# Performance work log

Measured on AMD Instinct MI355X. Metric: run time of the kernel, lower is better.

## Reference

```python
import jax, jax.numpy as jnp
import numpy as np

DIM = 1024
HEADS = 8


def setup_inputs() -> dict:
    key = jax.random.key(0)
    ks = jax.random.split(key, 8)
    b, n, m, nc, d = 2, 1024, 4, 1024, DIM
    x = jax.random.normal(ks[0], (b, n, d), dtype=jnp.float32)
    context = jax.random.normal(ks[1], (b, m, nc, d), dtype=jnp.float32)
    doc_similarities = jax.random.normal(ks[2], (b, m), dtype=jnp.float32)
    # learned params (Linear weights stored as [in, out] for x @ W)
    s = 1.0 / np.sqrt(d)
    Wq = jax.random.uniform(ks[3], (d, d), minval=-s, maxval=s, dtype=jnp.float32)
    Wkv = jax.random.uniform(ks[4], (d, 2 * d), minval=-s, maxval=s, dtype=jnp.float32)
    Wout = jax.random.uniform(ks[5], (d, d), minval=-s, maxval=s, dtype=jnp.float32)
    bout = jax.random.uniform(ks[6], (d,), minval=-s, maxval=s, dtype=jnp.float32)
    beta = jnp.array(1.0, dtype=jnp.float32)
    return {"x": x, "context": context, "doc_similarities": doc_similarities,
            "Wq": Wq, "Wkv": Wkv, "beta": beta, "Wout": Wout, "bout": bout}


def reference(x, context, doc_similarities, Wq, Wkv, beta, Wout, bout):
    b, n, dim = x.shape
    h = HEADS
    hd = dim // h
    scale = dim ** -0.5
    m, nc = context.shape[1], context.shape[2]

    # q: [b, h, n, hd]
    q = (x @ Wq).reshape(b, n, h, hd).transpose(0, 2, 1, 3)

    # flatten docs: [b, m*nc, dim]
    ctx = context.reshape(b, m * nc, dim)
    # doc similarity bias, repeated per token within each doc: [b, m*nc]
    sim = jnp.repeat(doc_similarities, nc, axis=1) * beta

    kv = ctx @ Wkv  # [b, L, 2*dim]
    k, v = jnp.split(kv, 2, axis=-1)
    k = k.reshape(b, m * nc, h, hd).transpose(0, 2, 1, 3)  # [b, h, L, hd]
    v = v.reshape(b, m * nc, h, hd).transpose(0, 2, 1, 3)

    dots = jnp.einsum('bhid,bhjd->bhij', q, k) * scale
    dots = dots + sim[:, None, None, :]
    attn = jax.nn.softmax(dots, axis=-1)
    out = jnp.einsum('bhij,bhjd->bhid', attn, v)
    out = out.transpose(0, 2, 1, 3).reshape(b, n, dim)
    return out @ Wout + bout
```

## Files before the change

kernel.cpp:

```cpp
#include <hip/hip_runtime.h>
#include <stdint.h>

typedef __attribute__((ext_vector_type(4))) float f32x4;
typedef __attribute__((ext_vector_type(8))) __bf16 bf16x8;
typedef __attribute__((ext_vector_type(2))) unsigned int u32x2;

__device__ __forceinline__ uint16_t f2bf(float f) {
  uint32_t u = __builtin_bit_cast(uint32_t, f);
  u += 0x7FFFu + ((u >> 16) & 1u);
  return (uint16_t)(u >> 16);
}

__device__ __forceinline__ float bf2f(uint16_t u) {
  uint32_t v = ((uint32_t)u) << 16;
  return __builtin_bit_cast(float, v);
}

__device__ __forceinline__ uint32_t cvtpk_bf16(float lo, float hi) {
  uint32_t r;
  asm("v_cvt_pk_bf16_f32 %0, %1, %2" : "=v"(r) : "v"(lo), "v"(hi));
  return r;
}

__device__ __forceinline__ void swap_half32(uint32_t& a, uint32_t& b) {
#if __has_builtin(__builtin_amdgcn_permlane32_swap)
  u32x2 r = __builtin_amdgcn_permlane32_swap(a, b, false, false);
  a = r[0]; b = r[1];
#else
  int lane = __builtin_amdgcn_mbcnt_hi(~0u, __builtin_amdgcn_mbcnt_lo(~0u, 0));
  uint32_t ax = (uint32_t)__shfl_xor((int)a, 32, 64);
  uint32_t bx = (uint32_t)__shfl_xor((int)b, 32, 64);
  uint32_t an = (lane < 32) ? a : bx;
  uint32_t bn = (lane < 32) ? ax : b;
  a = an; b = bn;
#endif
}

__device__ __forceinline__ void swap_half16(uint32_t& a, uint32_t& b) {
#if __has_builtin(__builtin_amdgcn_permlane16_swap)
  u32x2 r = __builtin_amdgcn_permlane16_swap(a, b, false, false);
  a = r[0]; b = r[1];
#else
  int lane = __builtin_amdgcn_mbcnt_hi(~0u, __builtin_amdgcn_mbcnt_lo(~0u, 0));
  uint32_t ax = (uint32_t)__shfl_xor((int)a, 16, 64);
  uint32_t bx = (uint32_t)__shfl_xor((int)b, 16, 64);
  uint32_t an = ((lane & 16) == 0) ? a : bx;
  uint32_t bn = ((lane & 16) == 0) ? ax : b;
  a = an; b = bn;
#endif
}

__device__ __forceinline__ void load_lds16(const uint16_t* g, uint16_t* l) {
  __builtin_amdgcn_global_load_lds((const __attribute__((address_space(1))) void*)g,
                                   (__attribute__((address_space(3))) void*)l, 16, 0, 0);
}

__global__ __launch_bounds__(256) void k_prep(const float* __restrict__ x,
                                              const float* __restrict__ ctx,
                                              const float* __restrict__ Wq,
                                              const float* __restrict__ Wkv,
                                              const float* __restrict__ Wout,
                                              uint16_t* __restrict__ xb,
                                              uint16_t* __restrict__ ctxb,
                                              uint16_t* __restrict__ wqt,
                                              uint16_t* __restrict__ wkvt,
                                              uint16_t* __restrict__ woutt,
                                              float qscale) {
  __shared__ float tile[32][33];
  int id = blockIdx.x;
  int tid = threadIdx.x;
  if (id < 10240) {
    const float* in;
    uint16_t* out;
    int j = id * 256 + tid;
    if (j < 524288) { in = x; out = xb; }
    else            { in = ctx; out = ctxb; j -= 524288; }
    float4 v = ((const float4*)in)[j];
    union { uint16_t u[4]; uint64_t q; } o;
    o.u[0] = f2bf(v.x); o.u[1] = f2bf(v.y); o.u[2] = f2bf(v.z); o.u[3] = f2bf(v.w);
    ((uint64_t*)out)[j] = o.q;
    return;
  }
  id -= 10240;
  const float* W;
  uint16_t* Wt;
  int N, n0, k0;
  float sc = 1.0f;
  if (id < 1024)      { W = Wq;   Wt = wqt;   N = 1024; sc = qscale;
                        n0 = (id & 31) * 32; k0 = (id >> 5) * 32; }
  else if (id < 2048) { W = Wout; Wt = woutt; N = 1024; id -= 1024;
                        n0 = (id & 31) * 32; k0 = (id >> 5) * 32; }
  else                { W = Wkv;  Wt = wkvt;  N = 2048; id -= 2048;
                        n0 = (id & 63) * 32; k0 = (id >> 6) * 32; }
  int c = tid & 31, r0 = tid >> 5;
#pragma unroll
  for (int i = 0; i < 4; i++) {
    int r = r0 + i * 8;
    tile[r][c] = W[(size_t)(k0 + r) * N + n0 + c];
  }
  __syncthreads();
#pragma unroll
  for (int i = 0; i < 4; i++) {
    int r = r0 + i * 8;
    Wt[(size_t)(n0 + r) * 1024 + k0 + c] = f2bf(tile[c][r] * sc);
  }
}

__global__ __launch_bounds__(256, 4) void k_gemm_fused(const uint16_t* __restrict__ ctxb,
                                                       const uint16_t* __restrict__ wkvt,
                                                       const uint16_t* __restrict__ xb,
                                                       const uint16_t* __restrict__ wqt,
                                                       uint16_t* __restrict__ kb,
                                                       uint16_t* __restrict__ vtb,
                                                       uint16_t* __restrict__ qb) {
  __shared__ uint16_t smem[16384];
  const int K = 1024;
  const int tid = threadIdx.x;
  const int lane = tid & 63, w = tid >> 6;
  const int quad = lane >> 4, l16 = lane & 15;
  const int wr = (w >> 1) * 64, wc = (w & 1) * 64;
  int id = blockIdx.x;
  int bx, by, isQ;
  const uint16_t *Ab, *Bb;
  if (id < 1024) {
    isQ = 0;
    int xcd = id & 7, t = id >> 3;
    by = (xcd << 3) + (t & 7);
    bx = t >> 3;
    Ab = ctxb + (size_t)by * 128 * K;
    Bb = wkvt + (size_t)bx * 128 * K;
  } else {
    isQ = 1; id -= 1024;
    int xcd = id & 7, t = id >> 3;
    by = (xcd << 1) + (t & 1);
    bx = t >> 1;
    Ab = xb + (size_t)by * 128 * K;
    Bb = wqt + (size_t)bx * 128 * K;
  }
  f32x4 acc[4][4] = {};
  const int rA = tid >> 2, slotA = tid & 3;
  const int rA1 = rA + 64;
  const int segA0 = (slotA ^ ((rA + (rA >> 2)) & 3)) * 8;
  const int segA1 = (slotA ^ ((rA1 + (rA1 >> 2)) & 3)) * 8;
  const uint16_t* gA0 = Ab + (size_t)rA * K + segA0;
  const uint16_t* gA1 = Ab + (size_t)rA1 * K + segA1;
  const uint16_t* gB0 = Bb + (size_t)rA * K + segA0;
  const uint16_t* gB1 = Bb + (size_t)rA1 * K + segA1;
  load_lds16(gA0, smem + tid * 8);
  load_lds16(gA1, smem + (tid + 256) * 8);
  load_lds16(gB0, smem + (tid + 512) * 8);
  load_lds16(gB1, smem + (tid + 768) * 8);
  for (int t = 0; t < 32; ++t) {
    const uint16_t* la = smem + (t & 1) * 8192;
    const uint16_t* lb = la + 4096;
    if (t < 31) {
      uint16_t* ln = smem + ((t + 1) & 1) * 8192;
      const int k1 = (t + 1) * 32;
      load_lds16(gA0 + k1, ln + tid * 8);
      load_lds16(gA1 + k1, ln + (tid + 256) * 8);
      load_lds16(gB0 + k1, ln + (tid + 512) * 8);
      load_lds16(gB1 + k1, ln + (tid + 768) * 8);
      asm volatile("s_waitcnt vmcnt(4)\n\ts_barrier" ::: "memory");
    } else {
      asm volatile("s_waitcnt vmcnt(0)\n\ts_barrier" ::: "memory");
    }
    bf16x8 af[4], bfr[4];
#pragma unroll
    for (int i = 0; i < 4; i++) {
      int R = wr + i * 16 + l16;
      int s = quad ^ ((R + (R >> 2)) & 3);
      af[i] = *(const bf16x8*)&la[R * 32 + s * 8];
    }
#pragma unroll
    for (int j = 0; j < 4; j++) {
      int R = wc + j * 16 + l16;
      int s = quad ^ ((R + (R >> 2)) & 3);
      bfr[j] = *(const bf16x8*)&lb[R * 32 + s * 8];
    }
    __builtin_amdgcn_s_setprio(1);
#pragma unroll
    for (int i = 0; i < 4; i++)
#pragma unroll
      for (int j = 0; j < 4; j++)
        acc[i][j] = __builtin_amdgcn_mfma_f32_16x16x32_bf16(af[i], bfr[j], acc[i][j], 0, 0, 0);
    __builtin_amdgcn_s_setprio(0);
    asm volatile("s_barrier" ::: "memory");
  }
  __syncthreads();
  if (isQ) {
#pragma unroll
    for (int i = 0; i < 4; i++)
#pragma unroll
      for (int j = 0; j < 4; j++) {
        size_t row = (size_t)by * 128 + wr + i * 16 + quad * 4;
        size_t col = (size_t)bx * 128 + wc + j * 16 + l16;
#pragma unroll
        for (int r = 0; r < 4; r++)
          qb[(row + r) * 1024 + col] = f2bf(acc[i][j][r]);
      }
  } else if (bx < 8) {
#pragma unroll
    for (int i = 0; i < 4; i++)
#pragma unroll
      for (int j = 0; j < 4; j++) {
        int rowg = by * 128 + wr + i * 16 + quad * 4;
        int bb = rowg >> 12, l = rowg & 4095;
        int c = wc + j * 16 + l16;
        uint16_t* dst = kb + (((size_t)(bb * 8 + bx) * 4096 + l) * 128 + c);
#pragma unroll
        for (int r = 0; r < 4; r++)
          dst[r * 128] = f2bf(acc[i][j][r]);
      }
  } else {
    const int bh = (by >> 5) * 8 + (bx - 8);
    const int lbase = (by & 31) * 128;
    uint16_t* vdst = vtb + (size_t)bh * 524288;
#pragma unroll
    for (int half = 0; half < 2; half++) {
      if (wr == half * 64) {
#pragma unroll
        for (int i = 0; i < 4; i++)
#pragma unroll
          for (int j = 0; j < 4; j++) {
            int rowl = i * 16 + quad * 4;
            int col = wc + j * 16 + l16;
            union { uint64_t q; uint16_t u[4]; } pk;
#pragma unroll
            for (int r = 0; r < 4; r++) pk.u[r] = f2bf(acc[i][j][r]);
            *(uint64_t*)&smem[col * 72 + rowl] = pk.q;
          }
      }
      __syncthreads();
      {
        int col = tid >> 1, rseg = (tid & 1) * 32;
        const uint16_t* src = &smem[col * 72 + rseg];
        uint16_t* d = vdst + (size_t)col * 4096 + lbase + half * 64 + rseg;
#pragma unroll
        for (int k = 0; k < 4; k++)
          ((uint4*)d)[k] = *(const uint4*)&src[k * 8];
      }
      __syncthreads();
    }
  }
}

__global__ __launch_bounds__(256) void k_gemm64(const uint16_t* __restrict__ A,
                                                const uint16_t* __restrict__ Bt,
                                                float* __restrict__ Cf,
                                                const float* __restrict__ bias,
                                                int M, int N, int K) {
  __shared__ uint16_t smem[16384];
  const int tid = threadIdx.x;
  const int lane = tid & 63, w = tid >> 6;
  const int quad = lane >> 4, l16 = lane & 15;
  const int wr = (w >> 1) * 32, wc = (w & 1) * 32;
  const size_t tr0 = (size_t)blockIdx.y * 64, tc0 = (size_t)blockIdx.x * 64;
  f32x4 acc[2][2] = {};
  const int rS = tid >> 3, sS = tid & 7;
  const int seg = (sS ^ (rS & 7)) * 8;
  const uint16_t* Ab = A + tr0 * K;
  const uint16_t* Bb = Bt + tc0 * K;
  const uint16_t* gA0 = Ab + (size_t)rS * K + seg;
  const uint16_t* gA1 = Ab + (size_t)(rS + 32) * K + seg;
  const uint16_t* gB0 = Bb + (size_t)rS * K + seg;
  const uint16_t* gB1 = Bb + (size_t)(rS + 32) * K + seg;
  const int NT = K >> 6;
  load_lds16(gA0, smem + tid * 8);
  load_lds16(gA1, smem + (tid + 256) * 8);
  load_lds16(gB0, smem + (tid + 512) * 8);
  load_lds16(gB1, smem + (tid + 768) * 8);
  for (int t = 0; t < NT; ++t) {
    const uint16_t* la = smem + (t & 1) * 8192;
    const uint16_t* lb = la + 4096;
    if (t < NT - 1) {
      uint16_t* ln = smem + ((t + 1) & 1) * 8192;
      const int k1 = (t + 1) * 64;
      load_lds16(gA0 + k1, ln + tid * 8);
      load_lds16(gA1 + k1, ln + (tid + 256) * 8);
      load_lds16(gB0 + k1, ln + (tid + 512) * 8);
      load_lds16(gB1 + k1, ln + (tid + 768) * 8);
      asm volatile("s_waitcnt vmcnt(4)\n\ts_barrier" ::: "memory");
    } else {
      asm volatile("s_waitcnt vmcnt(0)\n\ts_barrier" ::: "memory");
    }
    __builtin_amdgcn_s_setprio(1);
#pragma unroll
    for (int sub = 0; sub < 2; sub++) {
      const int kk = sub * 4 + quad;
      bf16x8 af[2], bfr[2];
#pragma unroll
      for (int i = 0; i < 2; i++) {
        int R = wr + i * 16 + l16;
        af[i] = *(const bf16x8*)&la[R * 64 + (kk ^ (R & 7)) * 8];
      }
#pragma unroll
      for (int j = 0; j < 2; j++) {
        int R = wc + j * 16 + l16;
        bfr[j] = *(const bf16x8*)&lb[R * 64 + (kk ^ (R & 7)) * 8];
      }
#pragma unroll
      for (int i = 0; i < 2; i++)
#pragma unroll
        for (int j = 0; j < 2; j++)
          acc[i][j] = __builtin_amdgcn_mfma_f32_16x16x32_bf16(af[i], bfr[j], acc[i][j], 0, 0, 0);
    }
    __builtin_amdgcn_s_setprio(0);
    asm volatile("s_barrier" ::: "memory");
  }
#pragma unroll
  for (int i = 0; i < 2; i++) {
#pragma unroll
    for (int j = 0; j < 2; j++) {
      size_t row = tr0 + wr + i * 16 + quad * 4;
      size_t col = tc0 + wc + j * 16 + l16;
#pragma unroll
      for (int r = 0; r < 4; r++)
        Cf[(row + r) * N + col] = acc[i][j][r] + bias[col];
    }
  }
}

__global__ __launch_bounds__(256) void k_attn(const uint16_t* __restrict__ q,
                                              const uint16_t* __restrict__ kb,
                                              const uint16_t* __restrict__ vt,
                                              const float* __restrict__ sims,
                                              const float* __restrict__ beta,
                                              uint16_t* __restrict__ po,
                                              float* __restrict__ pl) {
  __shared__ uint16_t Kl[2][8192];
  __shared__ uint16_t Vl[2][8192];
  const int idx = blockIdx.x;
  const int qbx = idx >> 6, g = idx & 63;
  const int h = g >> 3, b = (g >> 2) & 1, sp = g & 3;
  const int q0 = qbx * 128;
  const int tid = threadIdx.x, lane = tid & 63, w = tid >> 6;
  const int quad = lane >> 4, l16 = lane & 15;
  const float wsplit =
      __builtin_amdgcn_exp2f(sims[b * 4 + sp] * beta[0] * 1.44269504f);

  union { uint32_t u[4]; bf16x8 v; } Oc;
#pragma unroll
  for (int j = 0; j < 4; j++) Oc.u[j] = 0x3F803F80u;
  const bf16x8 onesf = Oc.v;

  bf16x8 qf[2][4];
#pragma unroll
  for (int rb = 0; rb < 2; rb++) {
    const uint16_t* qrow =
        q + ((size_t)(b * 1024 + q0 + w * 32 + rb * 16 + l16)) * 1024 + h * 128 + quad * 8;
#pragma unroll
    for (int ks = 0; ks < 4; ks++) qf[rb][ks] = *(const bf16x8*)(qrow + ks * 32);
  }
  f32x4 o[2][8] = {};
  f32x4 o9[2] = {};

  const uint16_t* kptr = kb + ((size_t)(b * 8 + h) * 4096 + sp * 1024) * 128;
  const uint16_t* vptr = vt + ((size_t)(b * 8 + h) * 128) * 4096 + sp * 1024;

#pragma unroll
  for (int ii = 0; ii < 4; ii++) {
    int g2 = tid + ii * 256;
    int row = g2 >> 4, seg = (g2 & 15) ^ (row & 15);
    load_lds16(kptr + row * 128 + seg * 8, &Kl[0][g2 * 8]);
  }
#pragma unroll
  for (int ii = 0; ii < 4; ii++) {
    int g2 = tid + ii * 256;
    int row = g2 >> 3, seg = (g2 & 7) ^ (row & 7);
    load_lds16(vptr + (size_t)row * 4096 + seg * 8, &Vl[0][g2 * 8]);
  }

  for (int c = 0; c < 16; c++) {
    const uint16_t* Kc = Kl[c & 1];
    const uint16_t* Vc = Vl[c & 1];
    if (c < 15) {
      const uint16_t* kn = kptr + 64 * 128;
      const uint16_t* vn = vptr + 64;
      uint16_t* Kd = Kl[(c + 1) & 1];
      uint16_t* Vd = Vl[(c + 1) & 1];
#pragma unroll
      for (int ii = 0; ii < 4; ii++) {
        int g2 = tid + ii * 256;
        int row = g2 >> 4, seg = (g2 & 15) ^ (row & 15);
        load_lds16(kn + row * 128 + seg * 8, Kd + g2 * 8);
      }
#pragma unroll
      for (int ii = 0; ii < 4; ii++) {
        int g2 = tid + ii * 256;
        int row = g2 >> 3, seg = (g2 & 7) ^ (row & 7);
        load_lds16(vn + (size_t)row * 4096 + seg * 8, Vd + g2 * 8);
      }
      asm volatile("s_waitcnt vmcnt(8)\n\ts_barrier" ::: "memory");
    } else {
      asm volatile("s_waitcnt vmcnt(0)\n\ts_barrier" ::: "memory");
    }
#pragma unroll
    for (int kh = 0; kh < 2; kh++) {
      f32x4 s[2][2] = {{{0.f,0.f,0.f,0.f},{0.f,0.f,0.f,0.f}},
                       {{0.f,0.f,0.f,0.f},{0.f,0.f,0.f,0.f}}};
      __builtin_amdgcn_s_setprio(1);
#pragma unroll
      for (int nb2 = 0; nb2 < 2; nb2++) {
        const int nb = kh * 2 + nb2;
#pragma unroll
        for (int ks = 0; ks < 4; ks++) {
          bf16x8 kf = *(const bf16x8*)&Kc[(nb * 16 + l16) * 128 + (((ks * 4 + quad) ^ l16) * 8)];
          s[nb2][0] = __builtin_amdgcn_mfma_f32_16x16x32_bf16(kf, qf[0][ks], s[nb2][0], 0, 0, 0);
          s[nb2][1] = __builtin_amdgcn_mfma_f32_16x16x32_bf16(kf, qf[1][ks], s[nb2][1], 0, 0, 0);
        }
      }
      __builtin_amdgcn_s_setprio(0);
      bf16x8 pa[2];
#pragma unroll
      for (int qh = 0; qh < 2; qh++) {
        uint32_t a0 = cvtpk_bf16(__builtin_amdgcn_exp2f(s[0][qh][0]),
                                 __builtin_amdgcn_exp2f(s[0][qh][1]));
        uint32_t a1 = cvtpk_bf16(__builtin_amdgcn_exp2f(s[0][qh][2]),
                                 __builtin_amdgcn_exp2f(s[0][qh][3]));
        uint32_t b0 = cvtpk_bf16(__builtin_amdgcn_exp2f(s[1][qh][0]),
                                 __builtin_amdgcn_exp2f(s[1][qh][1]));
        uint32_t b1 = cvtpk_bf16(__builtin_amdgcn_exp2f(s[1][qh][2]),
                                 __builtin_amdgcn_exp2f(s[1][qh][3]));
        swap_half32(a0, b0);
        swap_half16(a0, b0);
        swap_half32(a1, b1);
        swap_half16(a1, b1);
        union { uint32_t u[4]; bf16x8 v; } pk_;
        pk_.u[0] = a0; pk_.u[1] = a1; pk_.u[2] = b0; pk_.u[3] = b1;
        pa[qh] = pk_.v;
      }
      const int sq = ((kh * 4 + quad) ^ (l16 & 7)) * 8;
      __builtin_amdgcn_s_setprio(1);
#pragma unroll
      for (int nb = 0; nb < 8; nb++) {
        bf16x8 vf = *(const bf16x8*)&Vc[(nb * 16 + l16) * 64 + sq];
        o[0][nb] = __builtin_amdgcn_mfma_f32_16x16x32_bf16(pa[0], vf, o[0][nb], 0, 0, 0);
        o[1][nb] = __builtin_amdgcn_mfma_f32_16x16x32_bf16(pa[1], vf, o[1][nb], 0, 0, 0);
      }
      o9[0] = __builtin_amdgcn_mfma_f32_16x16x32_bf16(pa[0], onesf, o9[0], 0, 0, 0);
      o9[1] = __builtin_amdgcn_mfma_f32_16x16x32_bf16(pa[1], onesf, o9[1], 0, 0, 0);
      __builtin_amdgcn_s_setprio(0);
    }
    asm volatile("s_barrier" ::: "memory");
    kptr += 64 * 128;
    vptr += 64;
  }
  const int rowbase = (sp * 16 + b * 8 + h) * 1024 + q0 + w * 32;
#pragma unroll
  for (int rb = 0; rb < 2; rb++)
#pragma unroll
    for (int r = 0; r < 4; r++) {
      int row = rowbase + rb * 16 + quad * 4 + r;
#pragma unroll
      for (int nb = 0; nb < 8; nb++)
        po[(size_t)row * 128 + nb * 16 + l16] = f2bf(o[rb][nb][r] * wsplit);
      if (l16 == 0)
        pl[row] = o9[rb][r] * wsplit;
    }
}

__global__ __launch_bounds__(256) void k_merge(const uint16_t* __restrict__ po,
                                               const float* __restrict__ pl,
                                               uint16_t* __restrict__ attb) {
  const int bq = blockIdx.x;
  const int b = bq >> 10, qi = bq & 1023;
  const int t = threadIdx.x;
  const int h = t >> 5, d0 = (t & 31) * 4;
  const int bh = b * 8 + h;
  float den = 0.f;
  float acc[4] = {0.f, 0.f, 0.f, 0.f};
#pragma unroll
  for (int s = 0; s < 4; s++) {
    den += pl[(s * 16 + bh) * 1024 + qi];
    union { uint64_t q; uint16_t u[4]; } v;
    v.q = *(const uint64_t*)&po[(((size_t)(s * 16 + bh)) * 1024 + qi) * 128 + d0];
#pragma unroll
    for (int j = 0; j < 4; j++) acc[j] += bf2f(v.u[j]);
  }
  const float inv = 1.0f / den;
  union { uint64_t q; uint16_t u[4]; } o;
#pragma unroll
  for (int j = 0; j < 4; j++) o.u[j] = f2bf(acc[j] * inv);
  *(uint64_t*)&attb[((size_t)(b * 1024 + qi)) * 1024 + h * 128 + d0] = o.q;
}

extern "C" void kernel_launch(void* const* d_in, const int* in_sizes, int n_in,
                              void* d_out, int out_size, void* d_ws, size_t ws_size,
                              hipStream_t stream) {
  (void)in_sizes; (void)n_in; (void)out_size; (void)ws_size;
  const float* x    = (const float*)d_in[0];
  const float* ctx  = (const float*)d_in[1];
  const float* sims = (const float*)d_in[2];
  const float* Wq   = (const float*)d_in[3];
  const float* Wkv  = (const float*)d_in[4];
  const float* beta = (const float*)d_in[5];
  const float* Wout = (const float*)d_in[6];
  const float* bout = (const float*)d_in[7];
  float* out = (float*)d_out;

  char* ws = (char*)d_ws;
  uint16_t* xb    = (uint16_t*)(ws + 0);
  uint16_t* ctxb  = (uint16_t*)(ws + (4u << 20));
  uint16_t* wqt   = (uint16_t*)(ws + (20u << 20));
  uint16_t* wkvt  = (uint16_t*)(ws + (22u << 20));
  uint16_t* kb    = (uint16_t*)(ws + (32u << 20));
  uint16_t* vtb   = (uint16_t*)(ws + (48u << 20));
  float*    pl    = (float*)   (ws + (64u << 20));
  uint16_t* woutt = (uint16_t*)(ws + (68u << 20));
  uint16_t* qb    = (uint16_t*)(ws + (70u << 20));
  uint16_t* attb  = (uint16_t*)(ws + (74u << 20));
  uint16_t* po = (uint16_t*)(ws + 0);

  const float LOG2E = 1.44269504f;
  const float qscale = 0.03125f * LOG2E;

  k_prep<<<14336, 256, 0, stream>>>(x, ctx, Wq, Wkv, Wout, xb, ctxb, wqt, wkvt, woutt, qscale);
  k_gemm_fused<<<1152, 256, 0, stream>>>(ctxb, wkvt, xb, wqt, kb, vtb, qb);
  k_attn<<<512, 256, 0, stream>>>(qb, kb, vtb, sims, beta, po, pl);
  k_merge<<<2048, 256, 0, stream>>>(po, pl, attb);
  k_gemm64<<<dim3(16, 32), 256, 0, stream>>>(attb, woutt, out, bout, 2048, 1024, 1024);
}
```

Baseline: 208.1 us.

## Split fused GEMM into 256x256 KV GEMM with 4-stage pipeline and separate Q GEMM

The KV projection moves to its own kernel with 256x256 tiles, 512 threads, a 4-buffer LDS ring (128 KB) and a 3-deep prefetch, which raises arithmetic intensity and hides global latency. The Q projection becomes a separate launch reusing the old 128x128 code. This adds one kernel launch and serializes Q after KV instead of sharing a grid. The KV grid is 256 blocks at one block per CU, so wave-level occupancy drops and the epilogue writes through a larger LDS transpose.

```diff
diff --git a/kernel.cpp b/kernel.cpp
--- a/kernel.cpp
+++ b/kernel.cpp
@@ -106,13 +106,125 @@
   }
 }
 
-__global__ __launch_bounds__(256, 4) void k_gemm_fused(const uint16_t* __restrict__ ctxb,
-                                                       const uint16_t* __restrict__ wkvt,
-                                                       const uint16_t* __restrict__ xb,
-                                                       const uint16_t* __restrict__ wqt,
-                                                       uint16_t* __restrict__ kb,
-                                                       uint16_t* __restrict__ vtb,
-                                                       uint16_t* __restrict__ qb) {
+__global__ __launch_bounds__(512, 1) void k_gemm_kv(const uint16_t* __restrict__ ctxb,
+                                                    const uint16_t* __restrict__ wkvt,
+                                                    uint16_t* __restrict__ kb,
+                                                    uint16_t* __restrict__ vtb) {
+  __shared__ uint16_t smem[65536];
+  const int K = 1024;
+  const int tid = threadIdx.x;
+  const int lane = tid & 63, w = tid >> 6;
+  const int quad = lane >> 4, l16 = lane & 15;
+  const int wm = w >> 2, wn = w & 3;
+  const int wr = wm * 128, wc = wn * 64;
+  int id = blockIdx.x;
+  int xcd = id & 7, t0 = id >> 3;
+  int by = xcd + 8 * (t0 & 3);
+  int bx = t0 >> 2;
+  const uint16_t* Ab = ctxb + (size_t)by * 256 * K;
+  const uint16_t* Bb = wkvt + (size_t)bx * 256 * K;
+  f32x4 acc[8][4] = {};
+  const int rS = tid >> 2, sS = tid & 3;
+  const int rS1 = rS + 128;
+  const int seg0 = (sS ^ ((rS + (rS >> 2)) & 3)) * 8;
+  const int seg1 = (sS ^ ((rS1 + (rS1 >> 2)) & 3)) * 8;
+  const uint16_t* gA0 = Ab + (size_t)rS * K + seg0;
+  const uint16_t* gA1 = Ab + (size_t)rS1 * K + seg1;
+  const uint16_t* gB0 = Bb + (size_t)rS * K + seg0;
+  const uint16_t* gB1 = Bb + (size_t)rS1 * K + seg1;
+#define KV_STAGE(kt, buf)                                        \
+  {                                                              \
+    uint16_t* ba_ = smem + (buf) * 16384;                        \
+    const int k0_ = (kt) * 32;                                   \
+    load_lds16(gA0 + k0_, ba_ + tid * 8);                        \
+    load_lds16(gA1 + k0_, ba_ + 4096 + tid * 8);                 \
+    load_lds16(gB0 + k0_, ba_ + 8192 + tid * 8);                 \
+    load_lds16(gB1 + k0_, ba_ + 12288 + tid * 8);                \
+  }
+  KV_STAGE(0, 0)
+  KV_STAGE(1, 1)
+  KV_STAGE(2, 2)
+  for (int t = 0; t < 32; ++t) {
+    if (t < 30)      asm volatile("s_waitcnt vmcnt(8)\n\ts_barrier" ::: "memory");
+    else if (t == 30) asm volatile("s_waitcnt vmcnt(4)\n\ts_barrier" ::: "memory");
+    else             asm volatile("s_waitcnt vmcnt(0)\n\ts_barrier" ::: "memory");
+    if (t < 29) KV_STAGE(t + 3, (t + 3) & 3)
+    const uint16_t* la = smem + (t & 3) * 16384;
+    const uint16_t* lb = la + 8192;
+    bf16x8 af[8], bfr[4];
+#pragma unroll
+    for (int i = 0; i < 8; i++) {
+      int R = wr + i * 16 + l16;
+      int s = quad ^ ((R + (R >> 2)) & 3);
+      af[i] = *(const bf16x8*)&la[R * 32 + s * 8];
+    }
+#pragma unroll
+    for (int j = 0; j < 4; j++) {
+      int R = wc + j * 16 + l16;
+      int s = quad ^ ((R + (R >> 2)) & 3);
+      bfr[j] = *(const bf16x8*)&lb[R * 32 + s * 8];
+    }
+    __builtin_amdgcn_s_setprio(1);
+#pragma unroll
+    for (int i = 0; i < 8; i++)
+#pragma unroll
+      for (int j = 0; j < 4; j++)
+        acc[i][j] = __builtin_amdgcn_mfma_f32_16x16x32_bf16(af[i], bfr[j], acc[i][j], 0, 0, 0);
+    __builtin_amdgcn_s_setprio(0);
+  }
+#undef KV_STAGE
+  __syncthreads();
+  if (bx < 4) {
+#pragma unroll
+    for (int i = 0; i < 8; i++)
+#pragma unroll
+      for (int j = 0; j < 4; j++) {
+        int rowg = by * 256 + wr + i * 16 + quad * 4;
+        int bb = rowg >> 12, l = rowg & 4095;
+        int colg = bx * 256 + wc + j * 16 + l16;
+        int h = colg >> 7, c = colg & 127;
+        uint16_t* dst = kb + (((size_t)(bb * 8 + h) * 4096 + l) * 128 + c);
+#pragma unroll
+        for (int r = 0; r < 4; r++)
+          dst[r * 128] = f2bf(acc[i][j][r]);
+      }
+  } else {
+    const int vh = bx - 4;
+    const int bb = by >> 4;
+    const int lb0 = (by & 15) * 256;
+#pragma unroll
+    for (int hh = 0; hh < 2; hh++) {
+      if ((wn >> 1) == hh) {
+#pragma unroll
+        for (int i = 0; i < 8; i++)
+#pragma unroll
+          for (int j = 0; j < 4; j++) {
+            int d = (wn & 1) * 64 + j * 16 + l16;
+            int rowl = wr + i * 16 + quad * 4;
+            union { uint64_t q; uint16_t u[4]; } pk;
+#pragma unroll
+            for (int r = 0; r < 4; r++) pk.u[r] = f2bf(acc[i][j][r]);
+            *(uint64_t*)&smem[d * 264 + rowl] = pk.q;
+          }
+      }
+      __syncthreads();
+      {
+        const int bh = bb * 8 + vh * 2 + hh;
+        const int d = tid >> 2, ls = (tid & 3) * 64;
+        const uint16_t* src = &smem[d * 264 + ls];
+        uint16_t* vd = vtb + (size_t)bh * 524288 + (size_t)d * 4096 + lb0 + ls;
+#pragma unroll
+        for (int k = 0; k < 8; k++)
+          ((uint4*)vd)[k] = *(const uint4*)&src[k * 8];
+      }
+      __syncthreads();
+    }
+  }
+}
+
+__global__ __launch_bounds__(256, 4) void k_gemm_q(const uint16_t* __restrict__ xb,
+                                                   const uint16_t* __restrict__ wqt,
+                                                   uint16_t* __restrict__ qb) {
   __shared__ uint16_t smem[16384];
   const int K = 1024;
   const int tid = threadIdx.x;
@@ -120,23 +232,11 @@
   const int quad = lane >> 4, l16 = lane & 15;
   const int wr = (w >> 1) * 64, wc = (w & 1) * 64;
   int id = blockIdx.x;
-  int bx, by, isQ;
-  const uint16_t *Ab, *Bb;
-  if (id < 1024) {
-    isQ = 0;
-    int xcd = id & 7, t = id >> 3;
-    by = (xcd << 3) + (t & 7);
-    bx = t >> 3;
-    Ab = ctxb + (size_t)by * 128 * K;
-    Bb = wkvt + (size_t)bx * 128 * K;
-  } else {
-    isQ = 1; id -= 1024;
-    int xcd = id & 7, t = id >> 3;
-    by = (xcd << 1) + (t & 1);
-    bx = t >> 1;
-    Ab = xb + (size_t)by * 128 * K;
-    Bb = wqt + (size_t)bx * 128 * K;
-  }
+  int xcd = id & 7, t = id >> 3;
+  int by = (xcd << 1) + (t & 1);
+  int bx = t >> 1;
+  const uint16_t* Ab = xb + (size_t)by * 128 * K;
+  const uint16_t* Bb = wqt + (size_t)bx * 128 * K;
   f32x4 acc[4][4] = {};
   const int rA = tid >> 2, slotA = tid & 3;
   const int rA1 = rA + 64;
@@ -150,12 +250,12 @@
   load_lds16(gA1, smem + (tid + 256) * 8);
   load_lds16(gB0, smem + (tid + 512) * 8);
   load_lds16(gB1, smem + (tid + 768) * 8);
-  for (int t = 0; t < 32; ++t) {
-    const uint16_t* la = smem + (t & 1) * 8192;
+  for (int t2 = 0; t2 < 32; ++t2) {
+    const uint16_t* la = smem + (t2 & 1) * 8192;
     const uint16_t* lb = la + 4096;
-    if (t < 31) {
-      uint16_t* ln = smem + ((t + 1) & 1) * 8192;
-      const int k1 = (t + 1) * 32;
+    if (t2 < 31) {
+      uint16_t* ln = smem + ((t2 + 1) & 1) * 8192;
+      const int k1 = (t2 + 1) * 32;
       load_lds16(gA0 + k1, ln + tid * 8);
       load_lds16(gA1 + k1, ln + (tid + 256) * 8);
       load_lds16(gB0 + k1, ln + (tid + 512) * 8);
@@ -186,62 +286,16 @@
     __builtin_amdgcn_s_setprio(0);
     asm volatile("s_barrier" ::: "memory");
   }
-  __syncthreads();
-  if (isQ) {
-#pragma unroll
-    for (int i = 0; i < 4; i++)
-#pragma unroll
-      for (int j = 0; j < 4; j++) {
-        size_t row = (size_t)by * 128 + wr + i * 16 + quad * 4;
-        size_t col = (size_t)bx * 128 + wc + j * 16 + l16;
-#pragma unroll
-        for (int r = 0; r < 4; r++)
-          qb[(row + r) * 1024 + col] = f2bf(acc[i][j][r]);
-      }
-  } else if (bx < 8) {
-#pragma unroll
-    for (int i = 0; i < 4; i++)
-#pragma unroll
-      for (int j = 0; j < 4; j++) {
-        int rowg = by * 128 + wr + i * 16 + quad * 4;
-        int bb = rowg >> 12, l = rowg & 4095;
-        int c = wc + j * 16 + l16;
-        uint16_t* dst = kb + (((size_t)(bb * 8 + bx) * 4096 + l) * 128 + c);
-#pragma unroll
-        for (int r = 0; r < 4; r++)
-          dst[r * 128] = f2bf(acc[i][j][r]);
-      }
-  } else {
-    const int bh = (by >> 5) * 8 + (bx - 8);
-    const int lbase = (by & 31) * 128;
-    uint16_t* vdst = vtb + (size_t)bh * 524288;
-#pragma unroll
-    for (int half = 0; half < 2; half++) {
-      if (wr == half * 64) {
-#pragma unroll
-        for (int i = 0; i < 4; i++)
-#pragma unroll
-          for (int j = 0; j < 4; j++) {
-            int rowl = i * 16 + quad * 4;
-            int col = wc + j * 16 + l16;
-            union { uint64_t q; uint16_t u[4]; } pk;
-#pragma unroll
-            for (int r = 0; r < 4; r++) pk.u[r] = f2bf(acc[i][j][r]);
-            *(uint64_t*)&smem[col * 72 + rowl] = pk.q;
-          }
-      }
-      __syncthreads();
-      {
-        int col = tid >> 1, rseg = (tid & 1) * 32;
-        const uint16_t* src = &smem[col * 72 + rseg];
-        uint16_t* d = vdst + (size_t)col * 4096 + lbase + half * 64 + rseg;
-#pragma unroll
-        for (int k = 0; k < 4; k++)
-          ((uint4*)d)[k] = *(const uint4*)&src[k * 8];
-      }
-      __syncthreads();
-    }
-  }
+#pragma unroll
+  for (int i = 0; i < 4; i++)
+#pragma unroll
+    for (int j = 0; j < 4; j++) {
+      size_t row = (size_t)by * 128 + wr + i * 16 + quad * 4;
+      size_t col = (size_t)bx * 128 + wc + j * 16 + l16;
+#pragma unroll
+      for (int r = 0; r < 4; r++)
+        qb[(row + r) * 1024 + col] = f2bf(acc[i][j][r]);
+    }
 }
 
 __global__ __launch_bounds__(256) void k_gemm64(const uint16_t* __restrict__ A,
@@ -515,7 +569,8 @@
   const float qscale = 0.03125f * LOG2E;
 
   k_prep<<<14336, 256, 0, stream>>>(x, ctx, Wq, Wkv, Wout, xb, ctxb, wqt, wkvt, woutt, qscale);
-  k_gemm_fused<<<1152, 256, 0, stream>>>(ctxb, wkvt, xb, wqt, kb, vtb, qb);
+  k_gemm_kv<<<256, 512, 0, stream>>>(ctxb, wkvt, kb, vtb);
+  k_gemm_q<<<128, 256, 0, stream>>>(xb, wqt, qb);
   k_attn<<<512, 256, 0, stream>>>(qb, kb, vtb, sims, beta, po, pl);
   k_merge<<<2048, 256, 0, stream>>>(po, pl, attb);
   k_gemm64<<<dim3(16, 32), 256, 0, stream>>>(attb, woutt, out, bout, 2048, 1024, 1024);
```

Result: slower. 217.3 us (+4.4%).

## Fuse split-KV merge into attention kernel via last-block atomic counter

Applied to the files above, without the earlier changes.

Removes the separate merge kernel launch. Each attention block now increments a per-(query block, head, batch) counter after writing its partial output. The block that finishes last for a group reduces the four partials and writes the normalized bf16 result. The counters are zeroed in the prep kernel. This saves one launch and some DRAM round-trip latency, but adds atomics and fences, and the tail merge work runs on only a quarter of the blocks with a less coalesced per-thread access pattern.

```diff
diff --git a/kernel.cpp b/kernel.cpp
--- a/kernel.cpp
+++ b/kernel.cpp
@@ -65,10 +65,12 @@
                                               uint16_t* __restrict__ wqt,
                                               uint16_t* __restrict__ wkvt,
                                               uint16_t* __restrict__ woutt,
+                                              int* __restrict__ ctr,
                                               float qscale) {
   __shared__ float tile[32][33];
   int id = blockIdx.x;
   int tid = threadIdx.x;
+  if (id == 0 && tid < 128) ctr[tid] = 0;
   if (id < 10240) {
     const float* in;
     uint16_t* out;
@@ -326,9 +328,12 @@
                                               const float* __restrict__ sims,
                                               const float* __restrict__ beta,
                                               uint16_t* __restrict__ po,
-                                              float* __restrict__ pl) {
+                                              float* __restrict__ pl,
+                                              uint16_t* __restrict__ attb,
+                                              int* __restrict__ ctr) {
   __shared__ uint16_t Kl[2][8192];
   __shared__ uint16_t Vl[2][8192];
+  __shared__ int last_flag;
   const int idx = blockIdx.x;
   const int qbx = idx >> 6, g = idx & 63;
   const int h = g >> 3, b = (g >> 2) & 1, sp = g & 3;
@@ -457,31 +462,37 @@
       if (l16 == 0)
         pl[row] = o9[rb][r] * wsplit;
     }
-}
-
-__global__ __launch_bounds__(256) void k_merge(const uint16_t* __restrict__ po,
-                                               const float* __restrict__ pl,
-                                               uint16_t* __restrict__ attb) {
-  const int bq = blockIdx.x;
-  const int b = bq >> 10, qi = bq & 1023;
-  const int t = threadIdx.x;
-  const int h = t >> 5, d0 = (t & 31) * 4;
-  const int bh = b * 8 + h;
+  __threadfence();
+  __syncthreads();
+  if (tid == 0)
+    last_flag = (atomicAdd(&ctr[(qbx << 4) | (h << 1) | b], 1) == 3);
+  __syncthreads();
+  if (!last_flag) return;
+  __threadfence();
+  const int bh2 = b * 8 + h;
+  const int qi = q0 + (tid >> 1);
+  const int d0 = (tid & 1) * 64;
   float den = 0.f;
-  float acc[4] = {0.f, 0.f, 0.f, 0.f};
-#pragma unroll
-  for (int s = 0; s < 4; s++) {
-    den += pl[(s * 16 + bh) * 1024 + qi];
-    union { uint64_t q; uint16_t u[4]; } v;
-    v.q = *(const uint64_t*)&po[(((size_t)(s * 16 + bh)) * 1024 + qi) * 128 + d0];
-#pragma unroll
-    for (int j = 0; j < 4; j++) acc[j] += bf2f(v.u[j]);
-  }
+#pragma unroll
+  for (int s2 = 0; s2 < 4; s2++) den += pl[((s2 * 16 + bh2) << 10) + qi];
   const float inv = 1.0f / den;
-  union { uint64_t q; uint16_t u[4]; } o;
-#pragma unroll
-  for (int j = 0; j < 4; j++) o.u[j] = f2bf(acc[j] * inv);
-  *(uint64_t*)&attb[((size_t)(b * 1024 + qi)) * 1024 + h * 128 + d0] = o.q;
+  uint16_t* dstp = attb + ((size_t)(b * 1024 + qi)) * 1024 + h * 128 + d0;
+#pragma unroll
+  for (int dc = 0; dc < 64; dc += 8) {
+    float acc8[8] = {0.f, 0.f, 0.f, 0.f, 0.f, 0.f, 0.f, 0.f};
+#pragma unroll
+    for (int s2 = 0; s2 < 4; s2++) {
+      const uint16_t* src = po + (((size_t)(s2 * 16 + bh2) * 1024 + qi) * 128) + d0 + dc;
+      union { uint4 v; uint16_t u[8]; } ld;
+      ld.v = *(const uint4*)src;
+#pragma unroll
+      for (int j = 0; j < 8; j++) acc8[j] += bf2f(ld.u[j]);
+    }
+    union { uint4 v; uint16_t u[8]; } st;
+#pragma unroll
+    for (int j = 0; j < 8; j++) st.u[j] = f2bf(acc8[j] * inv);
+    *(uint4*)(dstp + dc) = st.v;
+  }
 }
 
 extern "C" void kernel_launch(void* const* d_in, const int* in_sizes, int n_in,
@@ -506,6 +517,7 @@
   uint16_t* kb    = (uint16_t*)(ws + (32u << 20));
   uint16_t* vtb   = (uint16_t*)(ws + (48u << 20));
   float*    pl    = (float*)   (ws + (64u << 20));
+  int*      ctr   = (int*)     (ws + (66u << 20));
   uint16_t* woutt = (uint16_t*)(ws + (68u << 20));
   uint16_t* qb    = (uint16_t*)(ws + (70u << 20));
   uint16_t* attb  = (uint16_t*)(ws + (74u << 20));
@@ -514,9 +526,8 @@
   const float LOG2E = 1.44269504f;
   const float qscale = 0.03125f * LOG2E;
 
-  k_prep<<<14336, 256, 0, stream>>>(x, ctx, Wq, Wkv, Wout, xb, ctxb, wqt, wkvt, woutt, qscale);
+  k_prep<<<14336, 256, 0, stream>>>(x, ctx, Wq, Wkv, Wout, xb, ctxb, wqt, wkvt, woutt, ctr, qscale);
   k_gemm_fused<<<1152, 256, 0, stream>>>(ctxb, wkvt, xb, wqt, kb, vtb, qb);
-  k_attn<<<512, 256, 0, stream>>>(qb, kb, vtb, sims, beta, po, pl);
-  k_merge<<<2048, 256, 0, stream>>>(po, pl, attb);
+  k_attn<<<512, 256, 0, stream>>>(qb, kb, vtb, sims, beta, po, pl, attb, ctr);
   k_gemm64<<<dim3(16, 32), 256, 0, stream>>>(attb, woutt, out, bout, 2048, 1024, 1024);
 }
```

After: 328.6 us. +57.9%, slower.

## Use 128x128 tiles with XCD-aware block mapping for output projection GEMM

Applied to the files above, without the earlier changes.

Replaces the generic 64x64-tile output GEMM with a specialized 128x128-tile kernel using a 32-wide K step, a 4x4 MFMA accumulator grid per wave, and a new LDS swizzle. Blocks are remapped so neighbouring row tiles land on the same XCD to share L2. This increases data reuse per block but launches only 128 blocks, leaving many CUs idle, and raises register pressure.

```diff
diff --git a/kernel.cpp b/kernel.cpp
--- a/kernel.cpp
+++ b/kernel.cpp
@@ -244,37 +244,41 @@
   }
 }
 
-__global__ __launch_bounds__(256) void k_gemm64(const uint16_t* __restrict__ A,
-                                                const uint16_t* __restrict__ Bt,
-                                                float* __restrict__ Cf,
-                                                const float* __restrict__ bias,
-                                                int M, int N, int K) {
+__global__ __launch_bounds__(256, 4) void k_gemm_out(const uint16_t* __restrict__ attb,
+                                                     const uint16_t* __restrict__ woutt,
+                                                     float* __restrict__ Cf,
+                                                     const float* __restrict__ bias) {
   __shared__ uint16_t smem[16384];
+  const int K = 1024;
   const int tid = threadIdx.x;
   const int lane = tid & 63, w = tid >> 6;
   const int quad = lane >> 4, l16 = lane & 15;
-  const int wr = (w >> 1) * 32, wc = (w & 1) * 32;
-  const size_t tr0 = (size_t)blockIdx.y * 64, tc0 = (size_t)blockIdx.x * 64;
-  f32x4 acc[2][2] = {};
-  const int rS = tid >> 3, sS = tid & 7;
-  const int seg = (sS ^ (rS & 7)) * 8;
-  const uint16_t* Ab = A + tr0 * K;
-  const uint16_t* Bb = Bt + tc0 * K;
-  const uint16_t* gA0 = Ab + (size_t)rS * K + seg;
-  const uint16_t* gA1 = Ab + (size_t)(rS + 32) * K + seg;
-  const uint16_t* gB0 = Bb + (size_t)rS * K + seg;
-  const uint16_t* gB1 = Bb + (size_t)(rS + 32) * K + seg;
-  const int NT = K >> 6;
+  const int wr = (w >> 1) * 64, wc = (w & 1) * 64;
+  int id = blockIdx.x;
+  int xcd = id & 7, t = id >> 3;
+  int by = (xcd << 1) + (t & 1);
+  int bx = t >> 1;
+  const uint16_t* Ab = attb + (size_t)by * 128 * K;
+  const uint16_t* Bb = woutt + (size_t)bx * 128 * K;
+  f32x4 acc[4][4] = {};
+  const int rA = tid >> 2, slotA = tid & 3;
+  const int rA1 = rA + 64;
+  const int segA0 = (slotA ^ ((rA + (rA >> 2)) & 3)) * 8;
+  const int segA1 = (slotA ^ ((rA1 + (rA1 >> 2)) & 3)) * 8;
+  const uint16_t* gA0 = Ab + (size_t)rA * K + segA0;
+  const uint16_t* gA1 = Ab + (size_t)rA1 * K + segA1;
+  const uint16_t* gB0 = Bb + (size_t)rA * K + segA0;
+  const uint16_t* gB1 = Bb + (size_t)rA1 * K + segA1;
   load_lds16(gA0, smem + tid * 8);
   load_lds16(gA1, smem + (tid + 256) * 8);
   load_lds16(gB0, smem + (tid + 512) * 8);
   load_lds16(gB1, smem + (tid + 768) * 8);
-  for (int t = 0; t < NT; ++t) {
-    const uint16_t* la = smem + (t & 1) * 8192;
+  for (int t2 = 0; t2 < 32; ++t2) {
+    const uint16_t* la = smem + (t2 & 1) * 8192;
     const uint16_t* lb = la + 4096;
-    if (t < NT - 1) {
-      uint16_t* ln = smem + ((t + 1) & 1) * 8192;
-      const int k1 = (t + 1) * 64;
+    if (t2 < 31) {
+      uint16_t* ln = smem + ((t2 + 1) & 1) * 8192;
+      const int k1 = (t2 + 1) * 32;
       load_lds16(gA0 + k1, ln + tid * 8);
       load_lds16(gA1 + k1, ln + (tid + 256) * 8);
       load_lds16(gB0 + k1, ln + (tid + 512) * 8);
@@ -283,41 +287,39 @@
     } else {
       asm volatile("s_waitcnt vmcnt(0)\n\ts_barrier" ::: "memory");
     }
+    bf16x8 af[4], bfr[4];
+#pragma unroll
+    for (int i = 0; i < 4; i++) {
+      int R = wr + i * 16 + l16;
+      int s = quad ^ ((R + (R >> 2)) & 3);
+      af[i] = *(const bf16x8*)&la[R * 32 + s * 8];
+    }
+#pragma unroll
+    for (int j = 0; j < 4; j++) {
+      int R = wc + j * 16 + l16;
+      int s = quad ^ ((R + (R >> 2)) & 3);
+      bfr[j] = *(const bf16x8*)&lb[R * 32 + s * 8];
+    }
     __builtin_amdgcn_s_setprio(1);
 #pragma unroll
-    for (int sub = 0; sub < 2; sub++) {
-      const int kk = sub * 4 + quad;
-      bf16x8 af[2], bfr[2];
-#pragma unroll
-      for (int i = 0; i < 2; i++) {
-        int R = wr + i * 16 + l16;
-        af[i] = *(const bf16x8*)&la[R * 64 + (kk ^ (R & 7)) * 8];
-      }
-#pragma unroll
-      for (int j = 0; j < 2; j++) {
-        int R = wc + j * 16 + l16;
-        bfr[j] = *(const bf16x8*)&lb[R * 64 + (kk ^ (R & 7)) * 8];
-      }
-#pragma unroll
-      for (int i = 0; i < 2; i++)
-#pragma unroll
-        for (int j = 0; j < 2; j++)
-          acc[i][j] = __builtin_amdgcn_mfma_f32_16x16x32_bf16(af[i], bfr[j], acc[i][j], 0, 0, 0);
-    }
+    for (int i = 0; i < 4; i++)
+#pragma unroll
+      for (int j = 0; j < 4; j++)
+        acc[i][j] = __builtin_amdgcn_mfma_f32_16x16x32_bf16(af[i], bfr[j], acc[i][j], 0, 0, 0);
     __builtin_amdgcn_s_setprio(0);
     asm volatile("s_barrier" ::: "memory");
   }
 #pragma unroll
-  for (int i = 0; i < 2; i++) {
-#pragma unroll
-    for (int j = 0; j < 2; j++) {
-      size_t row = tr0 + wr + i * 16 + quad * 4;
-      size_t col = tc0 + wc + j * 16 + l16;
+  for (int i = 0; i < 4; i++)
+#pragma unroll
+    for (int j = 0; j < 4; j++) {
+      size_t row = (size_t)by * 128 + wr + i * 16 + quad * 4;
+      size_t col = (size_t)bx * 128 + wc + j * 16 + l16;
+      float bv = bias[col];
 #pragma unroll
       for (int r = 0; r < 4; r++)
-        Cf[(row + r) * N + col] = acc[i][j][r] + bias[col];
-    }
-  }
+        Cf[(row + r) * 1024 + col] = acc[i][j][r] + bv;
+    }
 }
 
 __global__ __launch_bounds__(256) void k_attn(const uint16_t* __restrict__ q,
@@ -518,5 +520,5 @@
   k_gemm_fused<<<1152, 256, 0, stream>>>(ctxb, wkvt, xb, wqt, kb, vtb, qb);
   k_attn<<<512, 256, 0, stream>>>(qb, kb, vtb, sims, beta, po, pl);
   k_merge<<<2048, 256, 0, stream>>>(po, pl, attb);
-  k_gemm64<<<dim3(16, 32), 256, 0, stream>>>(attb, woutt, out, bout, 2048, 1024, 1024);
-}
+  k_gemm_out<<<128, 256, 0, stream>>>(attb, woutt, out, bout);
+}
```

Measured after the change: 222.0 us. 6.7% more time.
